# Performance work log

Hardware: AMD Instinct MI355X
Metric: run time of the kernel (lower is better)

The kernel has to match this reference:

```python
import jax, jax.numpy as jnp
import numpy as np

B, C, H, W = 8, 128, 128, 128
PLANES, K, STRIDE, PAD = 128, 3, 1, 1
BN_EPS = 1e-5


def setup_inputs() -> dict:
    key = jax.random.key(0)
    k1, k2, k3, k4 = jax.random.split(key, 4)
    x = jax.random.normal(k1, (B, C, H, W), jnp.float32)
    # ConvOffset2D: Conv2d(C, 2C, 3, pad=1, bias=False), weights ~ N(0, 0.01)
    w_off = jax.random.normal(k2, (2 * C, C, 3, 3), jnp.float32) * 0.01
    w_conv = jax.random.normal(k3, (PLANES, C, K, K), jnp.float32) * 0.05
    b_conv = jax.random.normal(k4, (PLANES,), jnp.float32) * 0.01
    gamma = jnp.ones((PLANES,), jnp.float32)
    beta = jnp.zeros((PLANES,), jnp.float32)
    return {"x": x, "w_off": w_off, "w_conv": w_conv, "b_conv": b_conv,
            "gamma": gamma, "beta": beta}


def _conv2d(x, w, stride, pad):
    return jax.lax.conv_general_dilated(
        x, w, window_strides=(stride, stride),
        padding=[(pad, pad), (pad, pad)],
        dimension_numbers=("NCHW", "OIHW", "NCHW"))


def _deform_sample(x, offsets):
    """x: (B,C,H,W); offsets: (B,2C,H,W) -> bilinear offset-sampled (B,C,H,W).
    Faithful to ConvOffset2D: raw reshape (b,2c,h,w) -> (b*c, h*w, 2),
    coords = offsets + meshgrid(i,j), clamp, bilinear interp."""
    b, c, h, w = x.shape
    off = offsets.reshape(b * c, h * w, 2)              # quirky but faithful reshape
    grid = jnp.stack(jnp.meshgrid(jnp.arange(h, dtype=x.dtype),
                                  jnp.arange(w, dtype=x.dtype),
                                  indexing="ij"), axis=-1).reshape(1, h * w, 2)
    coords = off + grid                                  # (b*c, h*w, 2)
    yc = jnp.clip(coords[..., 0], 0.0, h - 1.0)
    xc = jnp.clip(coords[..., 1], 0.0, w - 1.0)
    y0, y1 = jnp.floor(yc), jnp.ceil(yc)
    x0, x1 = jnp.floor(xc), jnp.ceil(xc)
    img = x.reshape(b * c, h * w)

    def gather(yy, xx):
        idx = (yy * w + xx).astype(jnp.int32)
        return jnp.take_along_axis(img, idx, axis=1)

    v_lt = gather(y0, x0)
    v_rb = gather(y1, x1)
    v_lb = gather(y0, x1)
    v_rt = gather(y1, x0)
    dy = yc - y0
    dx = xc - x0
    v_t = v_lt + (v_rt - v_lt) * dy   # interp along height
    v_b = v_lb + (v_rb - v_lb) * dy
    out = v_t + (v_b - v_t) * dx      # interp along width
    return out.reshape(b, c, h, w)


def reference(x, w_off, w_conv, b_conv, gamma, beta):
    offsets = _conv2d(x, w_off, 1, 1)                    # (B, 2C, H, W)
    x_off = _deform_sample(x, offsets)                   # (B, C, H, W)
    y = _conv2d(x_off, w_conv, STRIDE, PAD) + b_conv[None, :, None, None]
    y = jax.nn.relu(y)
    # BatchNorm2d in training mode: batch statistics, biased variance
    mean = y.mean(axis=(0, 2, 3), keepdims=True)
    var = jnp.square(y - mean).mean(axis=(0, 2, 3), keepdims=True)
    y = (y - mean) * jax.lax.rsqrt(var + BN_EPS)
    return y * gamma[None, :, None, None] + beta[None, :, None, None]
```

## Files before the change

### kernel.cpp

```cpp
#include <hip/hip_runtime.h>

#define B_   8
#define C_   128
#define H_   128
#define W_   128
#define HW_  16384

typedef short v8s __attribute__((ext_vector_type(8)));
typedef float v4f __attribute__((ext_vector_type(4)));

#define ROWB 4160

__device__ __forceinline__ float bf2f(unsigned short u) {
  unsigned int v = ((unsigned int)u) << 16;
  float f; __builtin_memcpy(&f, &v, 4); return f;
}
__device__ __forceinline__ unsigned short f2us(float f) {
  unsigned int u; __builtin_memcpy(&u, &f, 4);
  u += 0x7fffu + ((u >> 16) & 1u);
  return (unsigned short)(u >> 16);
}

__global__ __launch_bounds__(256) void pack_w(const float* __restrict__ w,
                                              unsigned short* __restrict__ pack,
                                              uint4* __restrict__ zb, int G) {
  if (blockIdx.x == 0) zb[threadIdx.x] = (uint4){0u, 0u, 0u, 0u};
  int idx = blockIdx.x * 256 + threadIdx.x;
  if (idx >= 20480 * G) return;
  int j  = idx & 7;
  int l  = (idx >> 3) & 63;
  int g  = (idx >> 9) % G;
  int t2 = idx / (512 * G);
  int pp = t2 % 5;
  int cc = t2 / 5;
  int oc = g * 16 + (l & 15);
  int kk = ((l >> 4) << 3) + j;
  int ic = (cc << 4) + (kk & 15);
  int rs = pp * 2 + (kk >> 4);
  float v = (rs < 9) ? w[(oc * C_ + ic) * 9 + rs] : 0.f;
  pack[idx] = f2us(v);
}

__global__ __launch_bounds__(256) void transpose_x(const float* __restrict__ x,
                                                   unsigned short* __restrict__ xt) {
  __shared__ alignas(16) unsigned short t[32 * 132];
  const int j0 = blockIdx.x * 32, i = blockIdx.y, b = blockIdx.z;
  const int tid = threadIdx.x;
  for (int e = tid; e < 128 * 32; e += 256) {
    int c = e >> 5, jj = e & 31;
    float v = x[((b * C_ + c) * H_ + i) * W_ + j0 + jj];
    t[jj * 132 + c] = f2us(v);
  }
  __syncthreads();
  for (int f = tid; f < 1024; f += 256) {
    int cg = f >> 7, g = f & 127;
    int j = g >> 2, c4 = (g & 3) << 2;
    uint2 v = *(const uint2*)&t[j * 132 + cg * 16 + c4];
    *(uint2*)(xt + ((size_t)(b * 8 + cg) * HW_ + i * W_ + j0 + j) * 16 + c4) = v;
  }
}

template <int MODE, int G>
__global__ __launch_bounds__(256) void conv_gemm(const unsigned short* __restrict__ xt,
                                                 const unsigned short* __restrict__ pack,
                                                 const float* __restrict__ bias,
                                                 const char* __restrict__ zb,
                                                 unsigned short* __restrict__ outp,
                                                 float* __restrict__ ps) {
  __shared__ alignas(16) char rawb[3 * ROWB];
  __shared__ float bs1[128], bs2[128];

  const int nb = blockIdx.x;
  int b, i, mt;
  {
    int xcd = nb & 7, r = nb >> 3;
    if (MODE == 0) { b = r >> 5; mt = (r >> 4) & 1; i = xcd * 16 + (r & 15); }
    else           { b = r >> 4; mt = 0;            i = xcd * 16 + (r & 15); }
  }
  const int tid  = threadIdx.x;
  const int lane = tid & 63, wid = tid >> 6;
  const int q = lane >> 4, n = lane & 15;
  const int wm = wid & 1, wn = wid >> 1;

  if (MODE == 1 && tid < 128) { bs1[tid] = 0.f; bs2[tid] = 0.f; }
  if (tid < 12) {
    int r = tid >> 2, rem = tid & 3, side = rem >> 1, h = rem & 1;
    *(uint4*)(rawb + r * ROWB + (side ? 129 * 32 : 0) + h * 16) = (uint4){0u,0u,0u,0u};
  }

  int boff[5];
#pragma unroll
  for (int pp = 0; pp < 5; ++pp) {
    int rs = pp * 2 + (q >> 1);
    if (rs > 8) rs = 8;
    int r = (rs >= 6) ? 2 : ((rs >= 3) ? 1 : 0);
    int s = rs - r * 3;
    boff[pp] = r * ROWB + s * 32 + (q & 1) * 16;
  }
  const int pcol = (wn * 64 + n) * 32;

  v4f acc[4][4];
#pragma unroll
  for (int a = 0; a < 4; ++a)
#pragma unroll
    for (int c = 0; c < 4; ++c) acc[a][c] = (v4f){0.f, 0.f, 0.f, 0.f};

  const v8s* packv = (const v8s*)pack;
  const int gbase = mt * 8 + wm * 4;

  v8s Acur[4];
  {
    const v8s* ap = packv + (0 * G + gbase) * 64 + lane;
#pragma unroll
    for (int fm = 0; fm < 4; ++fm) Acur[fm] = ap[fm * 64];
  }

  for (int cc = 0; cc < 8; ++cc) {
    __syncthreads();
    const char* ccbase = (const char*)xt + (size_t)(b * 8 + cc) * (HW_ * 32);
#pragma unroll
    for (int t = 0; t < 3; ++t) {
      int c = wid * 3 + t, r = c >> 2, k = c & 3;
      int ii = i + r - 1;
      const char* src = ((unsigned)ii < 128u)
                          ? ccbase + ii * 4096 + k * 1024 + lane * 16
                          : zb + lane * 16;
      __builtin_amdgcn_global_load_lds(
          (const __attribute__((address_space(1))) unsigned int*)src,
          (__attribute__((address_space(3))) unsigned int*)(rawb + r * ROWB + 32 + k * 1024),
          16, 0, 0);
    }
    __syncthreads();

#pragma unroll
    for (int pp = 0; pp < 5; ++pp) {
      v8s Anxt[4];
      const bool havenext = (pp < 4) || (cc < 7);
      if (havenext) {
        int ncc = (pp < 4) ? cc : cc + 1;
        int npp = (pp < 4) ? pp + 1 : 0;
        const v8s* ap = packv + ((ncc * 5 + npp) * G + gbase) * 64 + lane;
#pragma unroll
        for (int fm = 0; fm < 4; ++fm) Anxt[fm] = ap[fm * 64];
      }
      v8s Bf[4];
#pragma unroll
      for (int fn = 0; fn < 4; ++fn)
        Bf[fn] = *(const v8s*)(rawb + boff[pp] + pcol + fn * 512);
#pragma unroll
      for (int fm = 0; fm < 4; ++fm) {
#pragma unroll
        for (int fn = 0; fn < 4; ++fn)
          acc[fm][fn] = __builtin_amdgcn_mfma_f32_16x16x32_bf16(Acur[fm], Bf[fn],
                                                                acc[fm][fn], 0, 0, 0);
      }
      if (havenext) {
#pragma unroll
        for (int fm = 0; fm < 4; ++fm) Acur[fm] = Anxt[fm];
      }
    }
  }

  const int OC = G * 16;
  const int ob = (b * OC + mt * 128 + wm * 64) * HW_ + i * W_ + wn * 64;

  if (MODE == 0) {
#pragma unroll
    for (int fm = 0; fm < 4; ++fm)
#pragma unroll
      for (int fn = 0; fn < 4; ++fn)
#pragma unroll
        for (int rr = 0; rr < 4; ++rr)
          outp[ob + (fm * 16 + q * 4 + rr) * HW_ + fn * 16 + n] = f2us(acc[fm][fn][rr]);
  } else {
    float bv[4][4], s1a[4][4], s2a[4][4];
#pragma unroll
    for (int fm = 0; fm < 4; ++fm)
#pragma unroll
      for (int rr = 0; rr < 4; ++rr) {
        bv[fm][rr] = bias[wm * 64 + fm * 16 + q * 4 + rr];
        s1a[fm][rr] = 0.f; s2a[fm][rr] = 0.f;
      }
#pragma unroll
    for (int fm = 0; fm < 4; ++fm)
#pragma unroll
      for (int fn = 0; fn < 4; ++fn)
#pragma unroll
        for (int rr = 0; rr < 4; ++rr) {
          float v = acc[fm][fn][rr] + bv[fm][rr];
          v = fmaxf(v, 0.f);
          outp[ob + (fm * 16 + q * 4 + rr) * HW_ + fn * 16 + n] = f2us(v);
          s1a[fm][rr] += v; s2a[fm][rr] += v * v;
        }
#pragma unroll
    for (int fm = 0; fm < 4; ++fm)
#pragma unroll
      for (int rr = 0; rr < 4; ++rr) {
        float s1 = s1a[fm][rr], s2 = s2a[fm][rr];
#pragma unroll
        for (int m = 1; m < 16; m <<= 1) {
          s1 += __shfl_xor(s1, m);
          s2 += __shfl_xor(s2, m);
        }
        if (n == 0) {
          atomicAdd(&bs1[wm * 64 + fm * 16 + q * 4 + rr], s1);
          atomicAdd(&bs2[wm * 64 + fm * 16 + q * 4 + rr], s2);
        }
      }
    __syncthreads();
    if (tid < 128) {
      ps[nb * 128 + tid]          = bs1[tid];
      ps[131072 + nb * 128 + tid] = bs2[tid];
    }
  }
}

__global__ __launch_bounds__(256) void deform_t(const float* __restrict__ x,
                                                const unsigned short* __restrict__ offs,
                                                unsigned short* __restrict__ xofft) {
  __shared__ alignas(16) unsigned short t[128 * 132];
  const int i = blockIdx.x, b = blockIdx.y;
  const int tid = threadIdx.x;
  for (int e = tid; e < 16384; e += 256) {
    int c = e >> 7, j = e & 127;
    int qpix = (i << 7) + j;
    int oidx = (b << 22) + (c << 15) + 2 * qpix;
    unsigned int pr = *(const unsigned int*)(offs + oidx);
    float oy = bf2f((unsigned short)(pr & 0xffffu));
    float ox = bf2f((unsigned short)(pr >> 16));
    float yc = fminf(fmaxf(oy + (float)i, 0.f), 127.f);
    float xc = fminf(fmaxf(ox + (float)j, 0.f), 127.f);
    float y0f = floorf(yc), y1f = ceilf(yc);
    float x0f = floorf(xc), x1f = ceilf(xc);
    int y0 = (int)y0f, y1 = (int)y1f, x0 = (int)x0f, x1 = (int)x1f;
    const float* img = x + ((b * C_ + c) << 14);
    float v_lt = img[y0 * W_ + x0];
    float v_rb = img[y1 * W_ + x1];
    float v_lb = img[y0 * W_ + x1];
    float v_rt = img[y1 * W_ + x0];
    float dy = yc - y0f, dx = xc - x0f;
    float v_t = v_lt + (v_rt - v_lt) * dy;
    float v_b = v_lb + (v_rb - v_lb) * dy;
    float o   = v_t + (v_b - v_t) * dx;
    t[j * 132 + c] = f2us(o);
  }
  __syncthreads();
  for (int f = tid; f < 4096; f += 256) {
    int cg = f >> 9, g = f & 511;
    int j = g >> 2, c4 = (g & 3) << 2;
    uint2 v = *(const uint2*)&t[j * 132 + cg * 16 + c4];
    *(uint2*)(xofft + ((size_t)(b * 8 + cg) * HW_ + i * W_ + j) * 16 + c4) = v;
  }
}

__global__ __launch_bounds__(256) void bn_finalize(const float* __restrict__ ps,
                                                   const float* __restrict__ gamma,
                                                   const float* __restrict__ beta,
                                                   float* __restrict__ stats) {
  const int c = blockIdx.x, tid = threadIdx.x;
  float s1 = 0.f, s2 = 0.f;
  for (int k = tid; k < 1024; k += 256) {
    s1 += ps[k * 128 + c];
    s2 += ps[131072 + k * 128 + c];
  }
#pragma unroll
  for (int m = 32; m > 0; m >>= 1) {
    s1 += __shfl_down(s1, m);
    s2 += __shfl_down(s2, m);
  }
  __shared__ float l1[4], l2[4];
  int wid = tid >> 6;
  if ((tid & 63) == 0) { l1[wid] = s1; l2[wid] = s2; }
  __syncthreads();
  if (tid == 0) {
    s1 = l1[0] + l1[1] + l1[2] + l1[3];
    s2 = l2[0] + l2[1] + l2[2] + l2[3];
    const float invn = 1.f / 131072.f;
    float mean = s1 * invn;
    float var  = s2 * invn - mean * mean;
    float inv  = rsqrtf(var + 1e-5f);
    float sc = gamma[c] * inv;
    stats[c]       = sc;
    stats[128 + c] = beta[c] - mean * sc;
  }
}

__global__ __launch_bounds__(256) void bn_apply(const unsigned short* __restrict__ y,
                                                const float* __restrict__ stats,
                                                float* __restrict__ out) {
  int gid = blockIdx.x * 256 + threadIdx.x;
  int base = gid << 3;
  int c = (base >> 14) & 127;
  float sc = stats[c], sh = stats[128 + c];
  uint4 u = *(const uint4*)(y + base);
  const unsigned short* us = (const unsigned short*)&u;
  float4 o0, o1;
  o0.x = bf2f(us[0]) * sc + sh;  o0.y = bf2f(us[1]) * sc + sh;
  o0.z = bf2f(us[2]) * sc + sh;  o0.w = bf2f(us[3]) * sc + sh;
  o1.x = bf2f(us[4]) * sc + sh;  o1.y = bf2f(us[5]) * sc + sh;
  o1.z = bf2f(us[6]) * sc + sh;  o1.w = bf2f(us[7]) * sc + sh;
  ((float4*)out)[gid * 2]     = o0;
  ((float4*)out)[gid * 2 + 1] = o1;
}

extern "C" void kernel_launch(void* const* d_in, const int* in_sizes, int n_in,
                              void* d_out, int out_size, void* d_ws, size_t ws_size,
                              hipStream_t stream) {
  const float* x      = (const float*)d_in[0];
  const float* w_off  = (const float*)d_in[1];
  const float* w_conv = (const float*)d_in[2];
  const float* b_conv = (const float*)d_in[3];
  const float* gamma  = (const float*)d_in[4];
  const float* beta   = (const float*)d_in[5];
  float* out = (float*)d_out;

  char* ws = (char*)d_ws;
  unsigned short* x_t    = (unsigned short*)ws;
  unsigned short* xoff_t = (unsigned short*)ws;
  unsigned short* offs = (unsigned short*)(ws + 33554432);
  unsigned short* yws  = (unsigned short*)(ws + 33554432);
  float* ps    = (float*)(ws + 67108864);
  float* stats = (float*)(ws + 68157440);
  unsigned short* pack_off  = (unsigned short*)(ws + 100663296);
  unsigned short* pack_main = (unsigned short*)(ws + 101318656);
  char* zb = ws + 101646336;

  pack_w<<<80 * 16, 256, 0, stream>>>(w_off, pack_off, (uint4*)zb, 16);
  pack_w<<<80 * 8, 256, 0, stream>>>(w_conv, pack_main, (uint4*)zb, 8);
  transpose_x<<<dim3(4, 128, 8), 256, 0, stream>>>(x, x_t);
  conv_gemm<0, 16><<<2048, 256, 0, stream>>>(x_t, pack_off, nullptr, zb, offs, nullptr);
  deform_t<<<dim3(128, 8), 256, 0, stream>>>(x, offs, xoff_t);
  conv_gemm<1, 8><<<1024, 256, 0, stream>>>(xoff_t, pack_main, b_conv, zb, yws, ps);
  bn_finalize<<<128, 256, 0, stream>>>(ps, gamma, beta, stats);
  bn_apply<<<8192, 256, 0, stream>>>(yws, stats, out);
}
```

Before: 332.5 us.

## Compute two output rows per conv block with 512 threads; merge prep kernels

The implicit-GEMM conv blocks now cover two output rows with eight waves, staging four input rows in LDS instead of three per output row. Each staged input row therefore feeds more MFMA work, and the block count halves for both convolutions. The partial-stat count in bn_finalize is adjusted to match. The weight-pack and input-transpose kernels are also merged into one launch to cut launch overhead, at the cost of larger blocks that may lower occupancy and raise register pressure.

```diff
diff --git a/kernel.cpp b/kernel.cpp
--- a/kernel.cpp
+++ b/kernel.cpp
@@ -21,11 +21,38 @@
   return (unsigned short)(u >> 16);
 }
 
-__global__ __launch_bounds__(256) void pack_w(const float* __restrict__ w,
-                                              unsigned short* __restrict__ pack,
-                                              uint4* __restrict__ zb, int G) {
-  if (blockIdx.x == 0) zb[threadIdx.x] = (uint4){0u, 0u, 0u, 0u};
-  int idx = blockIdx.x * 256 + threadIdx.x;
+__global__ __launch_bounds__(256) void prep(const float* __restrict__ x,
+                                            unsigned short* __restrict__ xt,
+                                            const float* __restrict__ w_off,
+                                            const float* __restrict__ w_conv,
+                                            unsigned short* __restrict__ pack_off,
+                                            unsigned short* __restrict__ pack_main,
+                                            uint4* __restrict__ zb) {
+  __shared__ alignas(16) unsigned short t[32 * 132];
+  const int bid = blockIdx.x, tid = threadIdx.x;
+  if (bid < 4096) {
+    const int j0 = (bid & 3) * 32, i = (bid >> 2) & 127, b = bid >> 9;
+    for (int e = tid; e < 128 * 32; e += 256) {
+      int c = e >> 5, jj = e & 31;
+      float v = x[((b * C_ + c) * H_ + i) * W_ + j0 + jj];
+      t[jj * 132 + c] = f2us(v);
+    }
+    __syncthreads();
+    for (int f = tid; f < 1024; f += 256) {
+      int cg = f >> 7, g = f & 127;
+      int j = g >> 2, c4 = (g & 3) << 2;
+      uint2 v = *(const uint2*)&t[j * 132 + cg * 16 + c4];
+      *(uint2*)(xt + ((size_t)(b * 8 + cg) * HW_ + i * W_ + j0 + j) * 16 + c4) = v;
+    }
+    return;
+  }
+  const int pb = bid - 4096;
+  if (pb == 0) zb[tid] = (uint4){0u, 0u, 0u, 0u};
+  const float* w;
+  unsigned short* pack;
+  int G, idx;
+  if (pb < 1280) { w = w_off;  pack = pack_off;  G = 16; idx = pb * 256 + tid; }
+  else           { w = w_conv; pack = pack_main; G = 8;  idx = (pb - 1280) * 256 + tid; }
   if (idx >= 20480 * G) return;
   int j  = idx & 7;
   int l  = (idx >> 3) & 63;
@@ -41,49 +68,31 @@
   pack[idx] = f2us(v);
 }
 
-__global__ __launch_bounds__(256) void transpose_x(const float* __restrict__ x,
-                                                   unsigned short* __restrict__ xt) {
-  __shared__ alignas(16) unsigned short t[32 * 132];
-  const int j0 = blockIdx.x * 32, i = blockIdx.y, b = blockIdx.z;
-  const int tid = threadIdx.x;
-  for (int e = tid; e < 128 * 32; e += 256) {
-    int c = e >> 5, jj = e & 31;
-    float v = x[((b * C_ + c) * H_ + i) * W_ + j0 + jj];
-    t[jj * 132 + c] = f2us(v);
-  }
-  __syncthreads();
-  for (int f = tid; f < 1024; f += 256) {
-    int cg = f >> 7, g = f & 127;
-    int j = g >> 2, c4 = (g & 3) << 2;
-    uint2 v = *(const uint2*)&t[j * 132 + cg * 16 + c4];
-    *(uint2*)(xt + ((size_t)(b * 8 + cg) * HW_ + i * W_ + j0 + j) * 16 + c4) = v;
-  }
-}
-
 template <int MODE, int G>
-__global__ __launch_bounds__(256) void conv_gemm(const unsigned short* __restrict__ xt,
+__global__ __launch_bounds__(512) void conv_gemm(const unsigned short* __restrict__ xt,
                                                  const unsigned short* __restrict__ pack,
                                                  const float* __restrict__ bias,
                                                  const char* __restrict__ zb,
                                                  unsigned short* __restrict__ outp,
                                                  float* __restrict__ ps) {
-  __shared__ alignas(16) char rawb[3 * ROWB];
+  __shared__ alignas(16) char rawb[4 * ROWB];
   __shared__ float bs1[128], bs2[128];
 
   const int nb = blockIdx.x;
-  int b, i, mt;
+  int b, ip, mt;
   {
     int xcd = nb & 7, r = nb >> 3;
-    if (MODE == 0) { b = r >> 5; mt = (r >> 4) & 1; i = xcd * 16 + (r & 15); }
-    else           { b = r >> 4; mt = 0;            i = xcd * 16 + (r & 15); }
-  }
+    if (MODE == 0) { b = r >> 4; mt = (r >> 3) & 1; ip = xcd * 8 + (r & 7); }
+    else           { b = r >> 3; mt = 0;            ip = xcd * 8 + (r & 7); }
+  }
+  const int i0 = ip * 2;
   const int tid  = threadIdx.x;
   const int lane = tid & 63, wid = tid >> 6;
   const int q = lane >> 4, n = lane & 15;
-  const int wm = wid & 1, wn = wid >> 1;
+  const int wr = wid & 1, wm = (wid >> 1) & 1, wn = wid >> 2;
 
   if (MODE == 1 && tid < 128) { bs1[tid] = 0.f; bs2[tid] = 0.f; }
-  if (tid < 12) {
+  if (tid < 16) {
     int r = tid >> 2, rem = tid & 3, side = rem >> 1, h = rem & 1;
     *(uint4*)(rawb + r * ROWB + (side ? 129 * 32 : 0) + h * 16) = (uint4){0u,0u,0u,0u};
   }
@@ -93,9 +102,9 @@
   for (int pp = 0; pp < 5; ++pp) {
     int rs = pp * 2 + (q >> 1);
     if (rs > 8) rs = 8;
-    int r = (rs >= 6) ? 2 : ((rs >= 3) ? 1 : 0);
-    int s = rs - r * 3;
-    boff[pp] = r * ROWB + s * 32 + (q & 1) * 16;
+    int dr = (rs >= 6) ? 2 : ((rs >= 3) ? 1 : 0);
+    int s = rs - dr * 3;
+    boff[pp] = (wr + dr) * ROWB + s * 32 + (q & 1) * 16;
   }
   const int pcol = (wn * 64 + n) * 32;
 
@@ -119,9 +128,9 @@
     __syncthreads();
     const char* ccbase = (const char*)xt + (size_t)(b * 8 + cc) * (HW_ * 32);
 #pragma unroll
-    for (int t = 0; t < 3; ++t) {
-      int c = wid * 3 + t, r = c >> 2, k = c & 3;
-      int ii = i + r - 1;
+    for (int t = 0; t < 2; ++t) {
+      int c = wid * 2 + t, r = c >> 2, k = c & 3;
+      int ii = i0 + r - 1;
       const char* src = ((unsigned)ii < 128u)
                           ? ccbase + ii * 4096 + k * 1024 + lane * 16
                           : zb + lane * 16;
@@ -162,7 +171,7 @@
   }
 
   const int OC = G * 16;
-  const int ob = (b * OC + mt * 128 + wm * 64) * HW_ + i * W_ + wn * 64;
+  const int ob = (b * OC + mt * 128 + wm * 64) * HW_ + (i0 + wr) * W_ + wn * 64;
 
   if (MODE == 0) {
 #pragma unroll
@@ -259,7 +268,7 @@
                                                    float* __restrict__ stats) {
   const int c = blockIdx.x, tid = threadIdx.x;
   float s1 = 0.f, s2 = 0.f;
-  for (int k = tid; k < 1024; k += 256) {
+  for (int k = tid; k < 512; k += 256) {
     s1 += ps[k * 128 + c];
     s2 += ps[131072 + k * 128 + c];
   }
@@ -325,12 +334,11 @@
   unsigned short* pack_main = (unsigned short*)(ws + 101318656);
   char* zb = ws + 101646336;
 
-  pack_w<<<80 * 16, 256, 0, stream>>>(w_off, pack_off, (uint4*)zb, 16);
-  pack_w<<<80 * 8, 256, 0, stream>>>(w_conv, pack_main, (uint4*)zb, 8);
-  transpose_x<<<dim3(4, 128, 8), 256, 0, stream>>>(x, x_t);
-  conv_gemm<0, 16><<<2048, 256, 0, stream>>>(x_t, pack_off, nullptr, zb, offs, nullptr);
+  prep<<<6016, 256, 0, stream>>>(x, x_t, w_off, w_conv, pack_off, pack_main,
+                                 (uint4*)zb);
+  conv_gemm<0, 16><<<1024, 512, 0, stream>>>(x_t, pack_off, nullptr, zb, offs, nullptr);
   deform_t<<<dim3(128, 8), 256, 0, stream>>>(x, offs, xoff_t);
-  conv_gemm<1, 8><<<1024, 256, 0, stream>>>(xoff_t, pack_main, b_conv, zb, yws, ps);
+  conv_gemm<1, 8><<<512, 512, 0, stream>>>(xoff_t, pack_main, b_conv, zb, yws, ps);
   bn_finalize<<<128, 256, 0, stream>>>(ps, gamma, beta, stats);
   bn_apply<<<8192, 256, 0, stream>>>(yws, stats, out);
 }
```

After: 331.4 us. About the same (-0.3%).
